# Kernel tuning notes

Measured on AMD Instinct MI355X. Metric: run time of the kernel, lower is better.

## Reference

```python
import jax, jax.numpy as jnp
import numpy as np

B, C, H, W = 8, 64, 112, 112
F, KH, KW = 128, 3, 3
SPARSITY = 0.7  # fraction of kernel entries zeroed (Uniform connector)


def setup_inputs() -> dict:
    key = jax.random.key(0)
    k1, k2, k3 = jax.random.split(key, 3)
    inputs = jax.random.normal(k1, (B, C, H, W), dtype=jnp.float32)
    fan_in = C * KH * KW
    limit = float(np.sqrt(6.0 / (F + fan_in)))
    vals = jax.random.uniform(k2, (F, fan_in), minval=-limit, maxval=limit, dtype=jnp.float32)
    mask = (jax.random.uniform(k3, (F, fan_in)) >= SPARSITY).astype(jnp.float32)
    kernel = vals * mask  # dense representation of the sparse kernel
    return {"inputs": inputs, "kernel": kernel}


def _extract_patches(x, kh, kw):
    # x: [B, S1, S2, C]; VALID padding, stride 1, rate 1.
    # Matches tf.image.extract_patches depth ordering: (pi, pj) major, channel minor.
    Bb, S1, S2, Cc = x.shape
    o1, o2 = S1 - kh + 1, S2 - kw + 1
    pats = jnp.stack(
        [x[:, i:i + o1, j:j + o2, :] for i in range(kh) for j in range(kw)],
        axis=3,
    )  # [B, o1, o2, kh*kw, C]
    return pats.reshape(Bb, o1, o2, kh * kw * Cc)


def reference(inputs, kernel):
    # inputs: [B, C, H, W] (NCHW, per bias_add data_format and build())
    x = jnp.transpose(inputs, (0, 3, 2, 1))  # [B, W, H, C] (perm [0,3,2,1] in original)
    p = _extract_patches(x, KH, KW)          # [B, oW, oH, KH*KW*C]
    # spmm(kernel [F, K], im2col [K, B*oW*oH]) expressed as a single contraction
    out = jnp.einsum('bwhk,fk->bfwh', p, kernel)  # [B, F, oW, oH]
    return out
```

## Files before the change

### kernel.cpp

```cpp
#include <hip/hip_runtime.h>

typedef unsigned short u16;
typedef unsigned int u32;
typedef _Float16 f16x8 __attribute__((ext_vector_type(8)));
typedef float f32x16 __attribute__((ext_vector_type(16)));

#define B_ 8
#define C_ 64
#define H_ 112
#define W_ 112
#define HW_ 12544
#define F_ 128
#define OH_ 110
#define OW_ 110
#define OWOH 12100
#define NPOS 96800
#define KK_ 576
#define NT_ 384
#define NWGF 506
#define OCTSTRIDE 802816
#define AELEMS 73728
#define AHALF 36864

__device__ __forceinline__ void gl_lds16(const void* g, void* l) {
  __builtin_amdgcn_global_load_lds((const __attribute__((address_space(1))) void*)g,
                                   (__attribute__((address_space(3))) void*)l,
                                   16, 0, 0);
}

__global__ __launch_bounds__(256) void prep_all(const float* __restrict__ in,
                                                const float* __restrict__ k,
                                                u16* __restrict__ xT,
                                                u16* __restrict__ kT) {
  const int bid = blockIdx.x;
  const int tid = threadIdx.x;
  if (bid >= 896) {
    const int base = (bid - 896) * 2048;
#pragma unroll
    for (int t = 0; t < 8; ++t) {
      int idx = base + t * 256 + tid;
      int c = idx & 7;
      int f = (idx >> 3) & 127;
      int hf = (idx >> 10) & 1;
      int ko16 = idx >> 11;
      _Float16 h = (_Float16)k[f * KK_ + ko16 * 16 + hf * 8 + c];
      kT[idx] = __builtin_bit_cast(u16, h);
    }
    return;
  }
  __shared__ float tile[8][8][113];
  const int b = bid / 112;
  const int r = bid % 112;
  const int oct = r / 14;
  const int hs = (r % 14) * 8;

  for (int idx = tid; idx < 8 * 8 * 112; idx += 256) {
    int c = idx / 896;
    int rem = idx - c * 896;
    int h = rem / 112;
    int w = rem - h * 112;
    tile[c][h][w] = in[(((size_t)(b * 64 + oct * 8 + c)) * 112 + (hs + h)) * 112 + w];
  }
  __syncthreads();

  for (int idx = tid; idx < 896; idx += 256) {
    int w = idx >> 3;
    int h = idx & 7;
    f16x8 v;
#pragma unroll
    for (int c = 0; c < 8; ++c) v[c] = (_Float16)tile[c][h][w];
    size_t o = ((((size_t)oct * B_ + b) * W_ + w) * H_ + (hs + h)) * 8;
    *(f16x8*)(xT + o) = v;
  }
}

__global__ __launch_bounds__(256, 2) void conv_mfma(
    const u16* __restrict__ xT, const u16* __restrict__ kT,
    float* __restrict__ out) {
  __shared__ u16 lds[AHALF];

  const int tid = threadIdx.x;
  const int wave = tid >> 6;
  const int lane = tid & 63;
  const int l31 = lane & 31;
  const int hi = lane >> 5;

  const int wg = blockIdx.x;
  const int nblk = wg >> 1;
  const int fh = wg & 1;
  const int n0 = nblk * NT_ + wave * 32;

  int posOff[3];
#pragma unroll
  for (int ni = 0; ni < 3; ++ni) {
    int n = n0 + ni * 128 + l31;
    if (n >= NPOS) n = 0;
    int b = n / OWOH;
    int r = n - b * OWOH;
    int w = r / OH_;
    int h = r - w * OH_;
    posOff[ni] = ((b * W_ + w) * H_ + h) * 8;
  }

  f16x8 bcur[6];
#pragma unroll
  for (int ni = 0; ni < 3; ++ni)
#pragma unroll
    for (int t = 0; t < 2; ++t)
      bcur[ni * 2 + t] = *(const f16x8*)(xT + (t * 2 + hi) * OCTSTRIDE + posOff[ni]);

#pragma unroll
  for (int it = 0; it < 18; ++it) {
    const int m = it * 256 + tid;
    const int src = ((m >> 6) << 7) + (fh << 6) + (m & 63);
    gl_lds16(kT + src * 8, (char*)lds + m * 16);
  }
  __syncthreads();

  f32x16 acc[2][3] = {};

#pragma unroll
  for (int s = 0; s < 18; ++s) {
    f16x8 bnext[6];
    if (s < 17) {
      const int sn = s + 1;
      const int tapn = sn >> 1;
      const int halfn = sn & 1;
      const int in_ = tapn / 3;
      const int jn = tapn - in_ * 3;
      const int sShiftN = (in_ * H_ + jn) * 8;
#pragma unroll
      for (int ni = 0; ni < 3; ++ni)
#pragma unroll
        for (int t = 0; t < 2; ++t)
          bnext[ni * 2 + t] = *(const f16x8*)(xT + (halfn * 4 + t * 2 + hi) * OCTSTRIDE +
                                              posOff[ni] + sShiftN);
    }

    f16x8 ah[4];
#pragma unroll
    for (int t = 0; t < 2; ++t)
#pragma unroll
      for (int mi = 0; mi < 2; ++mi)
        ah[t * 2 + mi] = *(const f16x8*)&lds[((((s * 2 + t) * 2 + hi) << 6) + mi * 32 + l31) * 8];

#pragma unroll
    for (int t = 0; t < 2; ++t)
#pragma unroll
      for (int mi = 0; mi < 2; ++mi)
#pragma unroll
        for (int ni = 0; ni < 3; ++ni)
          acc[mi][ni] = __builtin_amdgcn_mfma_f32_32x32x16_f16(ah[t * 2 + mi], bcur[ni * 2 + t],
                                                               acc[mi][ni], 0, 0, 0);

    if (s < 17) {
#pragma unroll
      for (int q = 0; q < 6; ++q) bcur[q] = bnext[q];
    }
  }

#pragma unroll
  for (int ni = 0; ni < 3; ++ni) {
    int n = n0 + ni * 128 + l31;
    if (n >= NPOS) continue;
    int b = n / OWOH;
    int r = n - b * OWOH;
    int w = r / OH_;
    int h = r - w * OH_;
    float* op = out + ((size_t)(b * F_) * OW_ + w) * OH_ + h;
#pragma unroll
    for (int mi = 0; mi < 2; ++mi) {
      const int fbase = fh * 64 + mi * 32 + 4 * hi;
#pragma unroll
      for (int reg = 0; reg < 16; ++reg) {
        int f = fbase + (reg & 3) + 8 * (reg >> 2);
        op[(size_t)f * OWOH] = acc[mi][ni][reg];
      }
    }
  }
}

__global__ void naive_conv(const float* __restrict__ in, const float* __restrict__ ker,
                           float* __restrict__ out) {
  int idx = blockIdx.x * 256 + threadIdx.x;
  const int total = B_ * F_ * OW_ * OH_;
  if (idx >= total) return;
  int h = idx % OH_;
  int w = (idx / OH_) % OW_;
  int f = (idx / (OW_ * OH_)) % F_;
  int b = idx / (F_ * OW_ * OH_);
  float s = 0.f;
  for (int tap = 0; tap < 9; ++tap) {
    int i = tap / 3, j = tap % 3;
    const float* ip = in + ((size_t)b * C_ * H_ + (h + j)) * W_ + (w + i);
    const float* kp = ker + (size_t)f * KK_ + tap * C_;
    for (int c = 0; c < C_; ++c) s += ip[(size_t)c * HW_] * kp[c];
  }
  out[idx] = s;
}

extern "C" void kernel_launch(void* const* d_in, const int* in_sizes, int n_in,
                              void* d_out, int out_size, void* d_ws, size_t ws_size,
                              hipStream_t stream) {
  const float* in = (const float*)d_in[0];
  const float* ker = (const float*)d_in[1];
  float* out = (float*)d_out;

  const size_t xElems = (size_t)B_ * H_ * W_ * C_;
  const size_t need = (xElems + AELEMS) * 2;

  if (ws_size < need) {
    int total = B_ * F_ * OW_ * OH_;
    naive_conv<<<(total + 255) / 256, 256, 0, stream>>>(in, ker, out);
    return;
  }

  u16* xT = (u16*)d_ws;
  u16* kT = xT + xElems;

  prep_all<<<932, 256, 0, stream>>>(in, ker, xT, kT);
  conv_mfma<<<NWGF, 256, 0, stream>>>(xT, kT, out);
}
```

Before: 38.38 us.

## Stage input halo tile in LDS and stream weights from global in conv

The conv kernel now uses 512-thread workgroups (8 waves, two filter halves) per 384-position block instead of two separate workgroups. It stages a 10-column input halo tile for each channel half into double-buffered LDS, so the 9 taps reuse LDS data instead of re-reading global memory. Weights are now read straight from global (cached) memory instead of LDS. The trade-off is much larger LDS use (about 140KB across two buffers), which limits occupancy, and weight loads now come from cache rather than LDS.

```diff
diff --git a/kernel.cpp b/kernel.cpp
--- a/kernel.cpp
+++ b/kernel.cpp
@@ -17,10 +17,13 @@
 #define NPOS 96800
 #define KK_ 576
 #define NT_ 384
-#define NWGF 506
+#define NBLK 253
 #define OCTSTRIDE 802816
 #define AELEMS 73728
-#define AHALF 36864
+#define COLS 10
+#define COLE 896
+#define OCTE (COLS * COLE)
+#define BUFE (4 * OCTE)
 
 __device__ __forceinline__ void gl_lds16(const void* g, void* l) {
   __builtin_amdgcn_global_load_lds((const __attribute__((address_space(1))) void*)g,
@@ -74,94 +77,105 @@
   }
 }
 
-__global__ __launch_bounds__(256, 2) void conv_mfma(
+__global__ __launch_bounds__(512, 2) void conv_mfma(
     const u16* __restrict__ xT, const u16* __restrict__ kT,
     float* __restrict__ out) {
-  __shared__ u16 lds[AHALF];
+  __shared__ u16 lds[2 * BUFE];
 
   const int tid = threadIdx.x;
   const int wave = tid >> 6;
   const int lane = tid & 63;
   const int l31 = lane & 31;
   const int hi = lane >> 5;
-
-  const int wg = blockIdx.x;
-  const int nblk = wg >> 1;
-  const int fh = wg & 1;
-  const int n0 = nblk * NT_ + wave * 32;
-
-  int posOff[3];
+  const int fg = wave >> 2;
+  const int nw = wave & 3;
+
+  const int nblk = blockIdx.x;
+  const int n0b = nblk * NT_;
+  const int b0 = n0b / OWOH;
+  const int r0 = n0b - b0 * OWOH;
+  const int w0 = r0 / OH_;
+  const int g0 = b0 * W_ + w0;
+
+  int narr[3], lcb[3], hh[3];
 #pragma unroll
   for (int ni = 0; ni < 3; ++ni) {
-    int n = n0 + ni * 128 + l31;
-    if (n >= NPOS) n = 0;
-    int b = n / OWOH;
-    int r = n - b * OWOH;
+    int n = n0b + nw * 96 + ni * 32 + l31;
+    narr[ni] = n;
+    int nc = n < NPOS ? n : NPOS - 1;
+    int b = nc / OWOH;
+    int r = nc - b * OWOH;
     int w = r / OH_;
     int h = r - w * OH_;
-    posOff[ni] = ((b * W_ + w) * H_ + h) * 8;
-  }
-
-  f16x8 bcur[6];
-#pragma unroll
-  for (int ni = 0; ni < 3; ++ni)
-#pragma unroll
-    for (int t = 0; t < 2; ++t)
-      bcur[ni * 2 + t] = *(const f16x8*)(xT + (t * 2 + hi) * OCTSTRIDE + posOff[ni]);
-
-#pragma unroll
-  for (int it = 0; it < 18; ++it) {
-    const int m = it * 256 + tid;
-    const int src = ((m >> 6) << 7) + (fh << 6) + (m & 63);
-    gl_lds16(kT + src * 8, (char*)lds + m * 16);
-  }
+    lcb[ni] = b * W_ + w - g0;
+    hh[ni] = h;
+  }
+
+  auto STAGE = [&](int half, int d) {
+#pragma unroll
+    for (int it = 0; it < 9; ++it) {
+      int m = it * 512 + tid;
+      if (m < 4480) {
+        int oct4 = m / 1120;
+        int rest = m - oct4 * 1120;
+        const u16* src = xT + (half * 4 + oct4) * OCTSTRIDE + g0 * COLE + rest * 8;
+        gl_lds16(src, &lds[d * BUFE + oct4 * OCTE + rest * 8]);
+      }
+    }
+  };
+
+  f32x16 acc[2][3] = {};
+
+#define COMPUTE(TAP, HALF, D)                                                          \
+  {                                                                                    \
+    const int i_ = (TAP) / 3, j_ = (TAP) - i_ * 3;                                     \
+    f16x8 ah[4];                                                                       \
+    _Pragma("unroll") for (int t = 0; t < 2; ++t)                                      \
+        _Pragma("unroll") for (int mi = 0; mi < 2; ++mi)                               \
+            ah[t * 2 + mi] = *(const f16x8*)(kT +                                      \
+            ((((((TAP) * 4 + (HALF) * 2 + t) * 2 + hi) << 7) + fg * 64 + mi * 32 + l31) \
+             << 3));                                                                   \
+    f16x8 bh[6];                                                                       \
+    _Pragma("unroll") for (int ni = 0; ni < 3; ++ni)                                   \
+        _Pragma("unroll") for (int t = 0; t < 2; ++t)                                  \
+            bh[ni * 2 + t] = *(const f16x8*)&lds[(D) * BUFE + (t * 2 + hi) * OCTE +    \
+                                                 (lcb[ni] + i_) * COLE +               \
+                                                 (hh[ni] + j_) * 8];                   \
+    _Pragma("unroll") for (int t = 0; t < 2; ++t)                                      \
+        _Pragma("unroll") for (int mi = 0; mi < 2; ++mi)                               \
+            _Pragma("unroll") for (int ni = 0; ni < 3; ++ni)                           \
+                acc[mi][ni] = __builtin_amdgcn_mfma_f32_32x32x16_f16(                  \
+                    ah[t * 2 + mi], bh[ni * 2 + t], acc[mi][ni], 0, 0, 0);             \
+  }
+
+  STAGE(0, 0);
   __syncthreads();
 
-  f32x16 acc[2][3] = {};
-
-#pragma unroll
-  for (int s = 0; s < 18; ++s) {
-    f16x8 bnext[6];
-    if (s < 17) {
-      const int sn = s + 1;
-      const int tapn = sn >> 1;
-      const int halfn = sn & 1;
-      const int in_ = tapn / 3;
-      const int jn = tapn - in_ * 3;
-      const int sShiftN = (in_ * H_ + jn) * 8;
-#pragma unroll
-      for (int ni = 0; ni < 3; ++ni)
-#pragma unroll
-        for (int t = 0; t < 2; ++t)
-          bnext[ni * 2 + t] = *(const f16x8*)(xT + (halfn * 4 + t * 2 + hi) * OCTSTRIDE +
-                                              posOff[ni] + sShiftN);
-    }
-
-    f16x8 ah[4];
-#pragma unroll
-    for (int t = 0; t < 2; ++t)
-#pragma unroll
-      for (int mi = 0; mi < 2; ++mi)
-        ah[t * 2 + mi] = *(const f16x8*)&lds[((((s * 2 + t) * 2 + hi) << 6) + mi * 32 + l31) * 8];
-
-#pragma unroll
-    for (int t = 0; t < 2; ++t)
-#pragma unroll
-      for (int mi = 0; mi < 2; ++mi)
-#pragma unroll
-        for (int ni = 0; ni < 3; ++ni)
-          acc[mi][ni] = __builtin_amdgcn_mfma_f32_32x32x16_f16(ah[t * 2 + mi], bcur[ni * 2 + t],
-                                                               acc[mi][ni], 0, 0, 0);
-
-    if (s < 17) {
-#pragma unroll
-      for (int q = 0; q < 6; ++q) bcur[q] = bnext[q];
-    }
-  }
+  COMPUTE(0, 0, 0)
+  COMPUTE(1, 0, 0)
+  COMPUTE(2, 0, 0)
+  STAGE(1, 1);
+  COMPUTE(3, 0, 0)
+  COMPUTE(4, 0, 0)
+  COMPUTE(5, 0, 0)
+  COMPUTE(6, 0, 0)
+  COMPUTE(7, 0, 0)
+  COMPUTE(8, 0, 0)
+  __syncthreads();
+  COMPUTE(0, 1, 1)
+  COMPUTE(1, 1, 1)
+  COMPUTE(2, 1, 1)
+  COMPUTE(3, 1, 1)
+  COMPUTE(4, 1, 1)
+  COMPUTE(5, 1, 1)
+  COMPUTE(6, 1, 1)
+  COMPUTE(7, 1, 1)
+  COMPUTE(8, 1, 1)
+#undef COMPUTE
 
 #pragma unroll
   for (int ni = 0; ni < 3; ++ni) {
-    int n = n0 + ni * 128 + l31;
+    int n = narr[ni];
     if (n >= NPOS) continue;
     int b = n / OWOH;
     int r = n - b * OWOH;
@@ -170,7 +184,7 @@
     float* op = out + ((size_t)(b * F_) * OW_ + w) * OH_ + h;
 #pragma unroll
     for (int mi = 0; mi < 2; ++mi) {
-      const int fbase = fh * 64 + mi * 32 + 4 * hi;
+      const int fbase = fg * 64 + mi * 32 + 4 * hi;
 #pragma unroll
       for (int reg = 0; reg < 16; ++reg) {
         int f = fbase + (reg & 3) + 8 * (reg >> 2);
@@ -219,5 +233,5 @@
   u16* kT = xT + xElems;
 
   prep_all<<<932, 256, 0, stream>>>(in, ker, xT, kT);
-  conv_mfma<<<NWGF, 256, 0, stream>>>(xT, kT, out);
-}
+  conv_mfma<<<NBLK, 512, 0, stream>>>(xT, kT, out);
+}
```

Result: slower. 42.50 us (+10.7%).
